# Performance work log

Measured on AMD Instinct MI355X. Metric: run time of the kernel, lower is better.

## Reference

```python
import jax, jax.numpy as jnp
import numpy as np

B, L, D, H = 2, 2048, 1024, 16
hd = D // H
SCALE = hd ** -0.5
K = 3


def _dwconv(x_bcl, w, b):
    # x_bcl: [B, C, L]; w: [C, 1, K] depthwise; b: [C]
    y = jax.lax.conv_general_dilated(
        x_bcl, w, window_strides=(1,), padding=[((K - 1) // 2, (K - 1) // 2)],
        feature_group_count=x_bcl.shape[1],
        dimension_numbers=('NCH', 'OIH', 'NCH'))
    return y + b[None, :, None]


def setup_inputs() -> dict:
    key = jax.random.key(0)
    ks = jax.random.split(key, 11)
    def n(k, shape, s=0.02):
        return jax.random.normal(k, shape, dtype=jnp.float32) * s
    return {
        'x': jax.random.normal(ks[0], (B, L, D), dtype=jnp.float32),
        'wq': n(ks[1], (D, D)), 'wk': n(ks[2], (D, D)),
        'wv': n(ks[3], (D, D)), 'wo': n(ks[4], (D, D)),
        'cq_w': n(ks[5], (D, 1, K), 0.3), 'cq_b': n(ks[6], (D,)),
        'ck_w': n(ks[7], (D, 1, K), 0.3), 'ck_b': n(ks[8], (D,)),
        'cv_w': n(ks[9], (D, 1, K), 0.3), 'cv_b': n(ks[10], (D,)),
    }


def reference(x, wq, wk, wv, wo, cq_w, cq_b, ck_w, ck_b, cv_w, cv_b):
    # Linear projections (torch Linear: y = x @ W^T); note k scaled BEFORE conv
    q = jnp.einsum('bld,ed->ble', x, wq)
    k = jnp.einsum('bld,ed->ble', x, wk) * SCALE
    v = jnp.einsum('bld,ed->ble', x, wv)
    # Depthwise conv along sequence dim
    q = _dwconv(q.transpose(0, 2, 1), cq_w, cq_b).transpose(0, 2, 1)
    k = _dwconv(k.transpose(0, 2, 1), ck_w, ck_b).transpose(0, 2, 1)
    v = _dwconv(v.transpose(0, 2, 1), cv_w, cv_b).transpose(0, 2, 1)
    # Split heads -> [B, H, L, hd]
    q = q.reshape(B, L, H, hd).transpose(0, 2, 1, 3)
    k = k.reshape(B, L, H, hd).transpose(0, 2, 1, 3)
    v = v.reshape(B, L, H, hd).transpose(0, 2, 1, 3)
    sim = jnp.einsum('bhqd,bhkd->bhqk', q, k)
    causal = jnp.triu(jnp.ones((L, L), dtype=bool), k=1)
    sim = jnp.where(causal[None, None], -jnp.inf, sim)
    attn = jax.nn.softmax(sim, axis=-1)
    ctxt = jnp.einsum('bhqk,bhkd->bhqd', attn, v)
    out = ctxt.transpose(0, 2, 1, 3).reshape(B, L, D)
    out = jnp.einsum('bld,ed->ble', out, wo)
    return out, attn
```

## Files before the change

kernel.cpp:

```cpp
#include <hip/hip_runtime.h>
#include <hip/hip_bf16.h>


constexpr int B = 2, L = 2048, D = 1024, H = 16, HD = 64;
constexpr float SCALE = 0.125f;
constexpr int M_ROWS = B * L;

typedef short sh8 __attribute__((ext_vector_type(8)));
typedef float f32x4 __attribute__((ext_vector_type(4)));

__device__ __forceinline__ unsigned short f2bf(float f) {
  union { float f; unsigned u; } x; x.f = f;
  unsigned r = x.u + 0x7FFFu + ((x.u >> 16) & 1u);
  return (unsigned short)(r >> 16);
}
__device__ __forceinline__ float bf2f(unsigned short u) {
  union { unsigned u; float f; } x; x.u = ((unsigned)u) << 16;
  return x.f;
}

#define GLL16(gsrc, ldsbase)                                                  \
  __builtin_amdgcn_global_load_lds(                                           \
      (const __attribute__((address_space(1))) void*)(gsrc),                  \
      (__attribute__((address_space(3))) void*)(ldsbase), 16, 0, 0)

__global__ __launch_bounds__(256) void cast_x_bf16(const float* __restrict__ in,
                                                   unsigned short* __restrict__ out) {
  const size_t g = (size_t)blockIdx.x * 256 + threadIdx.x;
  const float4 a = *(const float4*)&in[g * 8];
  const float4 b = *(const float4*)&in[g * 8 + 4];
  ushort4 o0, o1;
  o0.x = f2bf(a.x); o0.y = f2bf(a.y); o0.z = f2bf(a.z); o0.w = f2bf(a.w);
  o1.x = f2bf(b.x); o1.y = f2bf(b.y); o1.z = f2bf(b.z); o1.w = f2bf(b.w);
  *(ushort4*)&out[g * 8] = o0;
  *(ushort4*)&out[g * 8 + 4] = o1;
}

__global__ __launch_bounds__(256) void cast_w4_bf16(
    const float* __restrict__ wq, const float* __restrict__ wk,
    const float* __restrict__ wv, const float* __restrict__ wo,
    unsigned short* __restrict__ out) {
  const int z = blockIdx.z;
  const float* src = (z == 0) ? wq : (z == 1) ? wk : (z == 2) ? wv : wo;
  unsigned short* dst = out + (size_t)z * 1024 * 1024;
  const size_t g = (size_t)blockIdx.x * 256 + threadIdx.x;
  const float4 a = *(const float4*)&src[g * 8];
  const float4 b = *(const float4*)&src[g * 8 + 4];
  ushort4 o0, o1;
  o0.x = f2bf(a.x); o0.y = f2bf(a.y); o0.z = f2bf(a.z); o0.w = f2bf(a.w);
  o1.x = f2bf(b.x); o1.y = f2bf(b.y); o1.z = f2bf(b.z); o1.w = f2bf(b.w);
  *(ushort4*)&dst[g * 8] = o0;
  *(ushort4*)&dst[g * 8 + 4] = o1;
}

template <bool BF16OUT>
__device__ __forceinline__ void gemm_lds_body(
    const unsigned short* __restrict__ A, const unsigned short* __restrict__ W,
    void* __restrict__ Y, float alpha) {
  __shared__ __align__(16) unsigned short As[128 * 64];
  __shared__ __align__(16) unsigned short Ws[128 * 64];
  const int tid = threadIdx.x;
  const int wave = tid >> 6, lane = tid & 63;
  const int m = lane & 15, kg = lane >> 4;
  const int m0 = blockIdx.y * 128, n0 = blockIdx.x * 128;
  const int wr = wave >> 1, wc = wave & 1;
  const int srow = lane >> 3;
  const int schunk = lane & 7;

  f32x4 acc[4][4];
#pragma unroll
  for (int i = 0; i < 4; ++i)
#pragma unroll
    for (int j = 0; j < 4; ++j) acc[i][j] = (f32x4){0.f, 0.f, 0.f, 0.f};

  const int sch = (schunk ^ srow) * 8;

  for (int k0 = 0; k0 < 1024; k0 += 64) {
#pragma unroll
    for (int c = 0; c < 4; ++c) {
      const int grp = wave * 4 + c;
      const int row = grp * 8 + srow;
      GLL16(A + (size_t)(m0 + row) * 1024 + k0 + sch, (char*)As + grp * 1024);
      GLL16(W + (size_t)(n0 + row) * 1024 + k0 + sch, (char*)Ws + grp * 1024);
    }
    __syncthreads();
    sh8 af[4][2], bfr[4][2];
#pragma unroll
    for (int i = 0; i < 4; ++i) {
      const int ra = wr * 64 + i * 16 + m;
      const int rb = wc * 64 + i * 16 + m;
      const int x7 = m & 7;
#pragma unroll
      for (int s = 0; s < 2; ++s) {
        const int ch = ((s * 4 + kg) ^ x7) * 8;
        af[i][s]  = *(const sh8*)&As[ra * 64 + ch];
        bfr[i][s] = *(const sh8*)&Ws[rb * 64 + ch];
      }
    }
#pragma unroll
    for (int s = 0; s < 2; ++s)
#pragma unroll
      for (int i = 0; i < 4; ++i)
#pragma unroll
        for (int j = 0; j < 4; ++j)
          acc[i][j] = __builtin_amdgcn_mfma_f32_16x16x32_bf16(af[i][s], bfr[j][s],
                                                             acc[i][j], 0, 0, 0);
    __syncthreads();
  }

  const int R = m0 + wr * 64, C = n0 + wc * 64;
#pragma unroll
  for (int i = 0; i < 4; ++i)
#pragma unroll
    for (int j = 0; j < 4; ++j)
#pragma unroll
      for (int reg = 0; reg < 4; ++reg) {
        const int row = R + i * 16 + kg * 4 + reg;
        const int col = C + j * 16 + m;
        const float v = acc[i][j][reg] * alpha;
        if constexpr (BF16OUT)
          ((unsigned short*)Y)[(size_t)row * 1024 + col] = f2bf(v);
        else
          ((float*)Y)[(size_t)row * 1024 + col] = v;
      }
}

__global__ __launch_bounds__(256) void proj_mfma(
    const unsigned short* __restrict__ xb, const unsigned short* __restrict__ wb4,
    unsigned short* __restrict__ qpre, unsigned short* __restrict__ kpre,
    unsigned short* __restrict__ vpre) {
  const int z = blockIdx.z;
  const unsigned short* W = wb4 + (size_t)z * 1024 * 1024;
  unsigned short* Yo = (z == 0) ? qpre : (z == 1) ? kpre : vpre;
  gemm_lds_body<true>(xb, W, Yo, (z == 1) ? SCALE : 1.0f);
}

__global__ __launch_bounds__(256) void outproj_mfma(
    const unsigned short* __restrict__ ctxtb, const unsigned short* __restrict__ wob,
    float* __restrict__ out) {
  gemm_lds_body<false>(ctxtb, wob, out, 1.0f);
}

__global__ __launch_bounds__(256) void dwconv_bf16(const unsigned short* __restrict__ in,
                                                   const float* __restrict__ w,
                                                   const float* __restrict__ bias,
                                                   unsigned short* __restrict__ out) {
  const int gid = blockIdx.x * 256 + threadIdx.x;
  const int d4 = gid % (D / 4);
  const int l = (gid / (D / 4)) % L;
  const int b = gid / ((D / 4) * L);
  const int d = d4 * 4;
  const size_t base = ((size_t)b * L + l) * D + d;
  const ushort4 cu = *(const ushort4*)&in[base];
  ushort4 pu = make_ushort4(0, 0, 0, 0), nu = make_ushort4(0, 0, 0, 0);
  if (l > 0) pu = *(const ushort4*)&in[base - D];
  if (l < L - 1) nu = *(const ushort4*)&in[base + D];
  float o0 = w[(d + 0) * 3 + 0] * bf2f(pu.x) + w[(d + 0) * 3 + 1] * bf2f(cu.x) + w[(d + 0) * 3 + 2] * bf2f(nu.x) + bias[d + 0];
  float o1 = w[(d + 1) * 3 + 0] * bf2f(pu.y) + w[(d + 1) * 3 + 1] * bf2f(cu.y) + w[(d + 1) * 3 + 2] * bf2f(nu.y) + bias[d + 1];
  float o2 = w[(d + 2) * 3 + 0] * bf2f(pu.z) + w[(d + 2) * 3 + 1] * bf2f(cu.z) + w[(d + 2) * 3 + 2] * bf2f(nu.z) + bias[d + 2];
  float o3 = w[(d + 3) * 3 + 0] * bf2f(pu.w) + w[(d + 3) * 3 + 1] * bf2f(cu.w) + w[(d + 3) * 3 + 2] * bf2f(nu.w) + bias[d + 3];
  ushort4 o;
  o.x = f2bf(o0); o.y = f2bf(o1); o.z = f2bf(o2); o.w = f2bf(o3);
  *(ushort4*)&out[base] = o;
}

__global__ __launch_bounds__(256) void dwconv_v_t(const unsigned short* __restrict__ in,
                                                  const float* __restrict__ w,
                                                  const float* __restrict__ bias,
                                                  unsigned short* __restrict__ vt) {
  const int l0 = blockIdx.x * 64;
  const int h = blockIdx.y, b = blockIdx.z;
  const int d0 = h * HD;
  __shared__ unsigned short T[64][72];
  const int tid = threadIdx.x;
  const int dq = (tid & 15) * 4, lr = tid >> 4;
#pragma unroll
  for (int pass = 0; pass < 4; ++pass) {
    const int l = l0 + pass * 16 + lr;
    const size_t base = ((size_t)b * L + l) * D + d0 + dq;
    const ushort4 cu = *(const ushort4*)&in[base];
    ushort4 pu = make_ushort4(0, 0, 0, 0), nu = make_ushort4(0, 0, 0, 0);
    if (l > 0) pu = *(const ushort4*)&in[base - D];
    if (l < L - 1) nu = *(const ushort4*)&in[base + D];
    const float c[4] = {bf2f(cu.x), bf2f(cu.y), bf2f(cu.z), bf2f(cu.w)};
    const float pp[4] = {bf2f(pu.x), bf2f(pu.y), bf2f(pu.z), bf2f(pu.w)};
    const float nn[4] = {bf2f(nu.x), bf2f(nu.y), bf2f(nu.z), bf2f(nu.w)};
#pragma unroll
    for (int j = 0; j < 4; ++j) {
      const int d = d0 + dq + j;
      float o = w[d * 3 + 0] * pp[j] + w[d * 3 + 1] * c[j] + w[d * 3 + 2] * nn[j] + bias[d];
      T[dq + j][pass * 16 + lr] = f2bf(o);
    }
  }
  __syncthreads();
  const int dd = tid >> 2, lq = (tid & 3) * 16;
  const size_t rbase = ((size_t)(b * H + h) * HD + dd) * L + l0 + lq;
#pragma unroll
  for (int i = 0; i < 16; i += 4) {
    ushort4 o;
    o.x = T[dd][lq + i + 0]; o.y = T[dd][lq + i + 1];
    o.z = T[dd][lq + i + 2]; o.w = T[dd][lq + i + 3];
    *(ushort4*)&vt[rbase + i] = o;
  }
}

__global__ __launch_bounds__(512) void flash_pv(
    const unsigned short* __restrict__ qb, const unsigned short* __restrict__ kb,
    const unsigned short* __restrict__ vt, float* __restrict__ linv_g,
    unsigned short* __restrict__ ctxtb) {
  const int p = blockIdx.x, h = blockIdx.y, b = blockIdx.z;
  const int tid = threadIdx.x;
  const int wave = tid >> 6, lane = tid & 63;
  const int wg = wave & 3, half = wave >> 2;
  const int m = lane & 15, kg = lane >> 4;

  __shared__ unsigned short P_sh[8][16 * 72];
  __shared__ float cpart[64 * 68];
  __shared__ float lpart[64];

  const size_t bh = (size_t)b * H + h;
  const unsigned short* qbase = qb + (size_t)b * L * D + h * HD;
  const unsigned short* kbase = kb + (size_t)b * L * D + h * HD;
  const unsigned short* vbase = vt + bh * HD * L;
  float* lbase = linv_g + bh * L;

  for (int which = 0; which < 2; ++which) {
    const int qt = which ? (31 - p) : p;
    const int q0 = qt * 64;
    const int r0 = q0 + wg * 16;
    const int crow = kg * 4;

    sh8 qf[2];
#pragma unroll
    for (int s = 0; s < 2; ++s)
      qf[s] = *(const sh8*)(qbase + (size_t)(r0 + m) * D + s * 32 + kg * 8);

    f32x4 cacc[4];
#pragma unroll
    for (int ct = 0; ct < 4; ++ct) cacc[ct] = (f32x4){0.f, 0.f, 0.f, 0.f};
    float lsum[4] = {0.f, 0.f, 0.f, 0.f};

    for (int kt = half; kt <= qt; kt += 2) {
      const int kcol0 = kt * 64;
#pragma unroll
      for (int ct = 0; ct < 4; ++ct) {
        f32x4 sacc = {0.f, 0.f, 0.f, 0.f};
#pragma unroll
        for (int s = 0; s < 2; ++s) {
          sh8 kf = *(const sh8*)(kbase + (size_t)(kcol0 + ct * 16 + m) * D + s * 32 + kg * 8);
          sacc = __builtin_amdgcn_mfma_f32_16x16x32_bf16(qf[s], kf, sacc, 0, 0, 0);
        }
        const int col = kcol0 + ct * 16 + m;
#pragma unroll
        for (int reg = 0; reg < 4; ++reg) {
          const int row = r0 + crow + reg;
          const float e = (col <= row) ? __expf(sacc[reg]) : 0.f;
          lsum[reg] += e;
          P_sh[wave][(crow + reg) * 72 + ct * 16 + m] = f2bf(e);
        }
      }
      sh8 pf[2];
#pragma unroll
      for (int s = 0; s < 2; ++s)
        pf[s] = *(const sh8*)&P_sh[wave][m * 72 + s * 32 + kg * 8];
#pragma unroll
      for (int ct = 0; ct < 4; ++ct) {
#pragma unroll
        for (int s = 0; s < 2; ++s) {
          sh8 vf = *(const sh8*)(vbase + (size_t)(ct * 16 + m) * L + kcol0 + s * 32 + kg * 8);
          cacc[ct] = __builtin_amdgcn_mfma_f32_16x16x32_bf16(pf[s], vf, cacc[ct], 0, 0, 0);
        }
      }
    }

#pragma unroll
    for (int reg = 0; reg < 4; ++reg) {
      float v = lsum[reg];
      v += __shfl_xor(v, 1); v += __shfl_xor(v, 2);
      v += __shfl_xor(v, 4); v += __shfl_xor(v, 8);
      lsum[reg] = v;
    }

    if (half == 1) {
      if (m == 0) {
#pragma unroll
        for (int reg = 0; reg < 4; ++reg) lpart[wg * 16 + crow + reg] = lsum[reg];
      }
#pragma unroll
      for (int ct = 0; ct < 4; ++ct)
#pragma unroll
        for (int reg = 0; reg < 4; ++reg)
          cpart[(wg * 16 + crow + reg) * 68 + ct * 16 + m] = cacc[ct][reg];
    }
    __syncthreads();
    if (half == 0) {
      float linv[4];
#pragma unroll
      for (int reg = 0; reg < 4; ++reg)
        linv[reg] = 1.0f / (lsum[reg] + lpart[wg * 16 + crow + reg]);
#pragma unroll
      for (int ct = 0; ct < 4; ++ct)
#pragma unroll
        for (int reg = 0; reg < 4; ++reg) {
          const float v = cacc[ct][reg] + cpart[(wg * 16 + crow + reg) * 68 + ct * 16 + m];
          ctxtb[(size_t)(b * L + r0 + crow + reg) * D + h * HD + ct * 16 + m] =
              f2bf(v * linv[reg]);
        }
      if (m == 0) {
#pragma unroll
        for (int reg = 0; reg < 4; ++reg) lbase[r0 + crow + reg] = linv[reg];
      }
    }
    __syncthreads();
  }
}

__global__ __launch_bounds__(256) void attn_write(
    const unsigned short* __restrict__ qb, const unsigned short* __restrict__ kb,
    const float* __restrict__ linv_g, float* __restrict__ attn) {
  const int tc = blockIdx.x, tr = blockIdx.y, bhz = blockIdx.z;
  const int b = bhz >> 4, h = bhz & 15;
  float* attnb = attn + (size_t)bhz * L * L;

  if (tc > tr) {
    const int t = threadIdx.x;
    const int r = tr * 128 + (t >> 1);
    float* rp = attnb + (size_t)r * L + tc * 128 + (t & 1) * 64;
    const float4 z4 = make_float4(0, 0, 0, 0);
#pragma unroll
    for (int i = 0; i < 16; ++i) *(float4*)&rp[i * 4] = z4;
    return;
  }

  const int tid = threadIdx.x;
  const int wave = tid >> 6, lane = tid & 63;
  const int m = lane & 15, kg = lane >> 4;
  const int wr = wave >> 1, wc = wave & 1;
  const unsigned short* qbase = qb + (size_t)b * L * D + h * HD;
  const unsigned short* kbase = kb + (size_t)b * L * D + h * HD;
  const float* lbase = linv_g + (size_t)bhz * L;
  const int row0 = tr * 128 + wr * 64, col0 = tc * 128 + wc * 64;

  sh8 qf[4][2];
#pragma unroll
  for (int i = 0; i < 4; ++i)
#pragma unroll
    for (int s = 0; s < 2; ++s)
      qf[i][s] = *(const sh8*)(qbase + (size_t)(row0 + i * 16 + m) * D + s * 32 + kg * 8);

  f32x4 acc[4][4];
#pragma unroll
  for (int i = 0; i < 4; ++i)
#pragma unroll
    for (int j = 0; j < 4; ++j) acc[i][j] = (f32x4){0.f, 0.f, 0.f, 0.f};

#pragma unroll
  for (int s = 0; s < 2; ++s)
#pragma unroll
    for (int j = 0; j < 4; ++j) {
      sh8 kf = *(const sh8*)(kbase + (size_t)(col0 + j * 16 + m) * D + s * 32 + kg * 8);
#pragma unroll
      for (int i = 0; i < 4; ++i)
        acc[i][j] = __builtin_amdgcn_mfma_f32_16x16x32_bf16(qf[i][s], kf, acc[i][j], 0, 0, 0);
    }

  const bool diag = (tc == tr);
#pragma unroll
  for (int i = 0; i < 4; ++i)
#pragma unroll
    for (int reg = 0; reg < 4; ++reg) {
      const int row = row0 + i * 16 + kg * 4 + reg;
      const float li = lbase[row];
      float* rowp = attnb + (size_t)row * L;
#pragma unroll
      for (int j = 0; j < 4; ++j) {
        const int col = col0 + j * 16 + m;
        float val = __expf(acc[i][j][reg]) * li;
        if (diag && col > row) val = 0.f;
        rowp[col] = val;
      }
    }
}

extern "C" void kernel_launch(void* const* d_in, const int* in_sizes, int n_in,
                              void* d_out, int out_size, void* d_ws, size_t ws_size,
                              hipStream_t stream) {
  const float* x    = (const float*)d_in[0];
  const float* wq   = (const float*)d_in[1];
  const float* wk   = (const float*)d_in[2];
  const float* wv   = (const float*)d_in[3];
  const float* wo   = (const float*)d_in[4];
  const float* cq_w = (const float*)d_in[5];
  const float* cq_b = (const float*)d_in[6];
  const float* ck_w = (const float*)d_in[7];
  const float* ck_b = (const float*)d_in[8];
  const float* cv_w = (const float*)d_in[9];
  const float* cv_b = (const float*)d_in[10];

  float* out  = (float*)d_out;
  float* attn = (float*)d_out + (size_t)B * L * D;

  const size_t bufN = (size_t)B * L * D;
  unsigned short* ws16 = (unsigned short*)d_ws;
  unsigned short* qpre  = ws16 + 0 * bufN;
  unsigned short* kpre  = ws16 + 1 * bufN;
  unsigned short* vpre  = ws16 + 2 * bufN;
  unsigned short* qb    = ws16 + 3 * bufN;
  unsigned short* kbb   = ws16 + 4 * bufN;
  unsigned short* vtb   = ws16 + 5 * bufN;
  unsigned short* ctxtb = ws16 + 6 * bufN;
  unsigned short* xb    = ws16 + 7 * bufN;
  unsigned short* wb4   = ws16 + 8 * bufN;
  float* linv_g = (float*)(ws16 + 9 * bufN);

  cast_x_bf16<<<2048, 256, 0, stream>>>(x, xb);
  cast_w4_bf16<<<dim3(512, 1, 4), 256, 0, stream>>>(wq, wk, wv, wo, wb4);
  proj_mfma<<<dim3(1024 / 128, M_ROWS / 128, 3), 256, 0, stream>>>(
      xb, wb4, qpre, kpre, vpre);
  const int convBlocks = (B * L * (D / 4)) / 256;
  dwconv_bf16<<<convBlocks, 256, 0, stream>>>(qpre, cq_w, cq_b, qb);
  dwconv_bf16<<<convBlocks, 256, 0, stream>>>(kpre, ck_w, ck_b, kbb);
  dwconv_v_t<<<dim3(L / 64, H, B), 256, 0, stream>>>(vpre, cv_w, cv_b, vtb);
  flash_pv<<<dim3(16, H, B), 512, 0, stream>>>(qb, kbb, vtb, linv_g, ctxtb);
  attn_write<<<dim3(16, 16, B * H), 256, 0, stream>>>(qb, kbb, linv_g, attn);
  outproj_mfma<<<dim3(1024 / 128, M_ROWS / 128, 1), 256, 0, stream>>>(
      ctxtb, wb4 + 3ull * 1024 * 1024, out);
}
```

Before: 833.7 us.

## Transpose MFMA operands for vectorized stores and double-buffer GEMM LDS

```diff
diff --git a/kernel.cpp b/kernel.cpp
--- a/kernel.cpp
+++ b/kernel.cpp
@@ -17,6 +17,11 @@
 __device__ __forceinline__ float bf2f(unsigned short u) {
   union { unsigned u; float f; } x; x.u = ((unsigned)u) << 16;
   return x.f;
+}
+__device__ __forceinline__ unsigned pack_bf16(float a, float b) {
+  unsigned r;
+  asm("v_cvt_pk_bf16_f32 %0, %1, %2" : "=v"(r) : "v"(a), "v"(b));
+  return r;
 }
 
 #define GLL16(gsrc, ldsbase)                                                  \
@@ -57,8 +62,8 @@
 __device__ __forceinline__ void gemm_lds_body(
     const unsigned short* __restrict__ A, const unsigned short* __restrict__ W,
     void* __restrict__ Y, float alpha) {
-  __shared__ __align__(16) unsigned short As[128 * 64];
-  __shared__ __align__(16) unsigned short Ws[128 * 64];
+  __shared__ __align__(16) unsigned short As[2][128 * 64];
+  __shared__ __align__(16) unsigned short Ws[2][128 * 64];
   const int tid = threadIdx.x;
   const int wave = tid >> 6, lane = tid & 63;
   const int m = lane & 15, kg = lane >> 4;
@@ -75,15 +80,22 @@
 
   const int sch = (schunk ^ srow) * 8;
 
-  for (int k0 = 0; k0 < 1024; k0 += 64) {
+  auto stage = [&](int buf, int k0) {
 #pragma unroll
     for (int c = 0; c < 4; ++c) {
       const int grp = wave * 4 + c;
       const int row = grp * 8 + srow;
-      GLL16(A + (size_t)(m0 + row) * 1024 + k0 + sch, (char*)As + grp * 1024);
-      GLL16(W + (size_t)(n0 + row) * 1024 + k0 + sch, (char*)Ws + grp * 1024);
-    }
-    __syncthreads();
+      GLL16(A + (size_t)(m0 + row) * 1024 + k0 + sch, (char*)&As[buf][0] + grp * 1024);
+      GLL16(W + (size_t)(n0 + row) * 1024 + k0 + sch, (char*)&Ws[buf][0] + grp * 1024);
+    }
+  };
+
+  stage(0, 0);
+  __syncthreads();
+
+  for (int t = 0; t < 16; ++t) {
+    const int cur = t & 1;
+    if (t < 15) stage(cur ^ 1, (t + 1) * 64);
     sh8 af[4][2], bfr[4][2];
 #pragma unroll
     for (int i = 0; i < 4; ++i) {
@@ -93,8 +105,8 @@
 #pragma unroll
       for (int s = 0; s < 2; ++s) {
         const int ch = ((s * 4 + kg) ^ x7) * 8;
-        af[i][s]  = *(const sh8*)&As[ra * 64 + ch];
-        bfr[i][s] = *(const sh8*)&Ws[rb * 64 + ch];
+        af[i][s]  = *(const sh8*)&As[cur][ra * 64 + ch];
+        bfr[i][s] = *(const sh8*)&Ws[cur][rb * 64 + ch];
       }
     }
 #pragma unroll
@@ -103,26 +115,31 @@
       for (int i = 0; i < 4; ++i)
 #pragma unroll
         for (int j = 0; j < 4; ++j)
-          acc[i][j] = __builtin_amdgcn_mfma_f32_16x16x32_bf16(af[i][s], bfr[j][s],
+          acc[i][j] = __builtin_amdgcn_mfma_f32_16x16x32_bf16(bfr[j][s], af[i][s],
                                                              acc[i][j], 0, 0, 0);
     __syncthreads();
   }
 
-  const int R = m0 + wr * 64, C = n0 + wc * 64;
-#pragma unroll
-  for (int i = 0; i < 4; ++i)
-#pragma unroll
-    for (int j = 0; j < 4; ++j)
-#pragma unroll
-      for (int reg = 0; reg < 4; ++reg) {
-        const int row = R + i * 16 + kg * 4 + reg;
-        const int col = C + j * 16 + m;
-        const float v = acc[i][j][reg] * alpha;
-        if constexpr (BF16OUT)
-          ((unsigned short*)Y)[(size_t)row * 1024 + col] = f2bf(v);
-        else
-          ((float*)Y)[(size_t)row * 1024 + col] = v;
-      }
+  const int R = m0 + wr * 64, C0 = n0 + wc * 64;
+#pragma unroll
+  for (int i = 0; i < 4; ++i) {
+    const int row = R + i * 16 + m;
+#pragma unroll
+    for (int j = 0; j < 4; ++j) {
+      const int col = C0 + j * 16 + kg * 4;
+      if constexpr (BF16OUT) {
+        uint2 o;
+        o.x = pack_bf16(acc[i][j][0] * alpha, acc[i][j][1] * alpha);
+        o.y = pack_bf16(acc[i][j][2] * alpha, acc[i][j][3] * alpha);
+        *(uint2*)&((unsigned short*)Y)[(size_t)row * 1024 + col] = o;
+      } else {
+        float4 o;
+        o.x = acc[i][j][0] * alpha; o.y = acc[i][j][1] * alpha;
+        o.z = acc[i][j][2] * alpha; o.w = acc[i][j][3] * alpha;
+        *(float4*)&((float*)Y)[(size_t)row * 1024 + col] = o;
+      }
+    }
+  }
 }
 
 __global__ __launch_bounds__(256) void proj_mfma(
@@ -228,36 +245,42 @@
     const int qt = which ? (31 - p) : p;
     const int q0 = qt * 64;
     const int r0 = q0 + wg * 16;
-    const int crow = kg * 4;
+    const int row_q = r0 + m;
 
     sh8 qf[2];
 #pragma unroll
     for (int s = 0; s < 2; ++s)
-      qf[s] = *(const sh8*)(qbase + (size_t)(r0 + m) * D + s * 32 + kg * 8);
+      qf[s] = *(const sh8*)(qbase + (size_t)row_q * D + s * 32 + kg * 8);
 
     f32x4 cacc[4];
 #pragma unroll
     for (int ct = 0; ct < 4; ++ct) cacc[ct] = (f32x4){0.f, 0.f, 0.f, 0.f};
-    float lsum[4] = {0.f, 0.f, 0.f, 0.f};
-
-    for (int kt = half; kt <= qt; kt += 2) {
-      const int kcol0 = kt * 64;
+    float lsum = 0.f;
+
+    auto do_tile = [&](int kcol0, bool mask) {
 #pragma unroll
       for (int ct = 0; ct < 4; ++ct) {
         f32x4 sacc = {0.f, 0.f, 0.f, 0.f};
 #pragma unroll
         for (int s = 0; s < 2; ++s) {
           sh8 kf = *(const sh8*)(kbase + (size_t)(kcol0 + ct * 16 + m) * D + s * 32 + kg * 8);
-          sacc = __builtin_amdgcn_mfma_f32_16x16x32_bf16(qf[s], kf, sacc, 0, 0, 0);
+          sacc = __builtin_amdgcn_mfma_f32_16x16x32_bf16(kf, qf[s], sacc, 0, 0, 0);
         }
-        const int col = kcol0 + ct * 16 + m;
+        float e[4];
 #pragma unroll
         for (int reg = 0; reg < 4; ++reg) {
-          const int row = r0 + crow + reg;
-          const float e = (col <= row) ? __expf(sacc[reg]) : 0.f;
-          lsum[reg] += e;
-          P_sh[wave][(crow + reg) * 72 + ct * 16 + m] = f2bf(e);
+          float v = __expf(sacc[reg]);
+          if (mask) {
+            const int col = kcol0 + ct * 16 + kg * 4 + reg;
+            v = (col <= row_q) ? v : 0.f;
+          }
+          e[reg] = v;
+          lsum += v;
         }
+        uint2 pk;
+        pk.x = pack_bf16(e[0], e[1]);
+        pk.y = pack_bf16(e[2], e[3]);
+        *(uint2*)&P_sh[wave][m * 72 + ct * 16 + kg * 4] = pk;
       }
       sh8 pf[2];
 #pragma unroll
@@ -268,48 +291,35 @@
 #pragma unroll
         for (int s = 0; s < 2; ++s) {
           sh8 vf = *(const sh8*)(vbase + (size_t)(ct * 16 + m) * L + kcol0 + s * 32 + kg * 8);
-          cacc[ct] = __builtin_amdgcn_mfma_f32_16x16x32_bf16(pf[s], vf, cacc[ct], 0, 0, 0);
+          cacc[ct] = __builtin_amdgcn_mfma_f32_16x16x32_bf16(vf, pf[s], cacc[ct], 0, 0, 0);
         }
       }
-    }
-
-#pragma unroll
-    for (int reg = 0; reg < 4; ++reg) {
-      float v = lsum[reg];
-      v += __shfl_xor(v, 1); v += __shfl_xor(v, 2);
-      v += __shfl_xor(v, 4); v += __shfl_xor(v, 8);
-      lsum[reg] = v;
-    }
+    };
+
+    for (int kt = half; kt < qt; kt += 2) do_tile(kt * 64, false);
+    if ((qt & 1) == half) do_tile(q0, true);
+
+    lsum += __shfl_xor(lsum, 16);
+    lsum += __shfl_xor(lsum, 32);
 
     if (half == 1) {
-      if (m == 0) {
-#pragma unroll
-        for (int reg = 0; reg < 4; ++reg) lpart[wg * 16 + crow + reg] = lsum[reg];
-      }
+      if (kg == 0) lpart[wg * 16 + m] = lsum;
 #pragma unroll
       for (int ct = 0; ct < 4; ++ct)
-#pragma unroll
-        for (int reg = 0; reg < 4; ++reg)
-          cpart[(wg * 16 + crow + reg) * 68 + ct * 16 + m] = cacc[ct][reg];
+        *(f32x4*)&cpart[(wg * 16 + m) * 68 + ct * 16 + kg * 4] = cacc[ct];
     }
     __syncthreads();
     if (half == 0) {
-      float linv[4];
-#pragma unroll
-      for (int reg = 0; reg < 4; ++reg)
-        linv[reg] = 1.0f / (lsum[reg] + lpart[wg * 16 + crow + reg]);
-#pragma unroll
-      for (int ct = 0; ct < 4; ++ct)
-#pragma unroll
-        for (int reg = 0; reg < 4; ++reg) {
-          const float v = cacc[ct][reg] + cpart[(wg * 16 + crow + reg) * 68 + ct * 16 + m];
-          ctxtb[(size_t)(b * L + r0 + crow + reg) * D + h * HD + ct * 16 + m] =
-              f2bf(v * linv[reg]);
-        }
-      if (m == 0) {
-#pragma unroll
-        for (int reg = 0; reg < 4; ++reg) lbase[r0 + crow + reg] = linv[reg];
-      }
+      const float inv = 1.0f / (lsum + lpart[wg * 16 + m]);
+#pragma unroll
+      for (int ct = 0; ct < 4; ++ct) {
+        const f32x4 cp = *(const f32x4*)&cpart[(wg * 16 + m) * 68 + ct * 16 + kg * 4];
+        uint2 o;
+        o.x = pack_bf16((cacc[ct][0] + cp[0]) * inv, (cacc[ct][1] + cp[1]) * inv);
+        o.y = pack_bf16((cacc[ct][2] + cp[2]) * inv, (cacc[ct][3] + cp[3]) * inv);
+        *(uint2*)&ctxtb[(size_t)(b * L + row_q) * D + h * HD + ct * 16 + kg * 4] = o;
+      }
+      if (kg == 0) lbase[row_q] = inv;
     }
     __syncthreads();
   }
@@ -361,25 +371,33 @@
       sh8 kf = *(const sh8*)(kbase + (size_t)(col0 + j * 16 + m) * D + s * 32 + kg * 8);
 #pragma unroll
       for (int i = 0; i < 4; ++i)
-        acc[i][j] = __builtin_amdgcn_mfma_f32_16x16x32_bf16(qf[i][s], kf, acc[i][j], 0, 0, 0);
+        acc[i][j] = __builtin_amdgcn_mfma_f32_16x16x32_bf16(kf, qf[i][s], acc[i][j], 0, 0, 0);
     }
 
   const bool diag = (tc == tr);
 #pragma unroll
-  for (int i = 0; i < 4; ++i)
-#pragma unroll
-    for (int reg = 0; reg < 4; ++reg) {
-      const int row = row0 + i * 16 + kg * 4 + reg;
-      const float li = lbase[row];
-      float* rowp = attnb + (size_t)row * L;
-#pragma unroll
-      for (int j = 0; j < 4; ++j) {
-        const int col = col0 + j * 16 + m;
-        float val = __expf(acc[i][j][reg]) * li;
-        if (diag && col > row) val = 0.f;
-        rowp[col] = val;
-      }
-    }
+  for (int i = 0; i < 4; ++i) {
+    const int row = row0 + i * 16 + m;
+    const float li = lbase[row];
+    float* rowp = attnb + (size_t)row * L;
+#pragma unroll
+    for (int j = 0; j < 4; ++j) {
+      const int cbase = col0 + j * 16 + kg * 4;
+      float4 o;
+      float v0 = __expf(acc[i][j][0]) * li;
+      float v1 = __expf(acc[i][j][1]) * li;
+      float v2 = __expf(acc[i][j][2]) * li;
+      float v3 = __expf(acc[i][j][3]) * li;
+      if (diag) {
+        v0 = (cbase + 0 <= row) ? v0 : 0.f;
+        v1 = (cbase + 1 <= row) ? v1 : 0.f;
+        v2 = (cbase + 2 <= row) ? v2 : 0.f;
+        v3 = (cbase + 3 <= row) ? v3 : 0.f;
+      }
+      o.x = v0; o.y = v1; o.z = v2; o.w = v3;
+      *(float4*)&rowp[cbase] = o;
+    }
+  }
 }
 
 extern "C" void kernel_launch(void* const* d_in, const int* in_sizes, int n_in,
```

New measurement: 855.5 us. +2.6%, slower.
